# Performance work log

Hardware: AMD Instinct MI355X
Metric: run time of the kernel (lower is better)

The kernel has to match this reference:

```python
import jax, jax.numpy as jnp
import numpy as np

H = 4          # n_head
DM = 512       # d_model
DK = 512       # d_k (hardcoded in module)
NL = 32        # num_landmarks
WS = 10        # window_size
EXT = WS // 2  # ext_len = 5
T = 2 * EXT + WS  # tile width = 20


def _ln(x, g, b, eps=1e-5):
    m = jnp.mean(x, axis=-1, keepdims=True)
    v = jnp.mean((x - m) ** 2, axis=-1, keepdims=True)
    return (x - m) / jnp.sqrt(v + eps) * g + b


def setup_inputs() -> dict:
    key = jax.random.key(0)
    ks = jax.random.split(key, 8)
    b, s = 8, 2000
    inp = {
        "X": jax.random.normal(ks[0], (b, s, DM), dtype=jnp.float32),
        "event_emb": jnp.zeros((1,), jnp.float32),
        "g": jnp.zeros((1,), jnp.float32),
        "mask": jnp.ones((b, s, 1), jnp.float32),
        "Wq": 0.02 * jax.random.normal(ks[1], (DM, H * DK), jnp.float32),
        "bq": jnp.zeros((H * DK,), jnp.float32),
        "Wk": 0.02 * jax.random.normal(ks[2], (DM, H * DK), jnp.float32),
        "bk": jnp.zeros((H * DK,), jnp.float32),
        "Wv": 0.02 * jax.random.normal(ks[3], (DM, H * DK), jnp.float32),
        "bv": jnp.zeros((H * DK,), jnp.float32),
        "Wo": 0.02 * jax.random.normal(ks[4], (H * DK, DM), jnp.float32),
        "bo": jnp.zeros((DM,), jnp.float32),
        "Wd": 0.02 * jax.random.normal(ks[5], (DM, H * NL), jnp.float32),
        "bd": jnp.zeros((H * NL,), jnp.float32),
        "lnl_g": jnp.ones((H * DK,), jnp.float32),
        "lnl_b": jnp.zeros((H * DK,), jnp.float32),
        "lns_g": jnp.ones((H * DK,), jnp.float32),
        "lns_b": jnp.zeros((H * DK,), jnp.float32),
    }
    return inp


def reference(X, event_emb, g, mask, Wq, bq, Wk, bk, Wv, bv, Wo, bo, Wd, bd,
              lnl_g, lnl_b, lns_g, lns_b):
    b, s, _ = X.shape
    G = s // WS  # number of windows
    scale = 1.0 / np.sqrt(DK)

    def split(x):  # [b,s,H*DK] -> [b,H,s,DK]
        return x.reshape(b, s, H, DK).transpose(0, 2, 1, 3)

    Q = split(X @ Wq + bq) * scale
    K = split(_ln(X @ Wk + bk, lnl_g, lnl_b))
    V = split(_ln(X @ Wv + bv, lnl_g, lnl_b))

    pad_mask = mask[..., 0] == 0  # [b,s] True where padded

    # landmark (Nystrom-style) compression
    hs = X @ Wd + bd  # [b,s,H*NL]
    hs = jnp.where(pad_mask[:, :, None], -jnp.inf, hs)
    hs = jax.nn.softmax(hs.astype(jnp.float32), axis=1).astype(X.dtype)
    hs = hs.reshape(b, s, H, NL).transpose(0, 2, 3, 1)  # [b,H,NL,s]
    K_c = jnp.einsum('bhls,bhsd->bhld', hs, K)  # [b,H,NL,DK]
    V_c = jnp.einsum('bhls,bhsd->bhld', hs, V)
    # dual_ln_s over flattened heads
    K_c = _ln(K_c.transpose(0, 2, 1, 3).reshape(b, NL, H * DK), lns_g, lns_b)
    K_c = K_c.reshape(b, NL, H, DK).transpose(0, 2, 1, 3)
    V_c = _ln(V_c.transpose(0, 2, 1, 3).reshape(b, NL, H * DK), lns_g, lns_b)
    V_c = V_c.reshape(b, NL, H, DK).transpose(0, 2, 1, 3)

    attn_compress = jnp.einsum('bhsd,bhld->bhsl', Q, K_c)  # [b,H,s,NL]

    # sliding-window chunked attention (v2 tiling)
    idx = jnp.arange(G)[:, None] * WS + jnp.arange(T)[None, :]  # [G,T]
    K_pad = jnp.pad(K, ((0, 0), (0, 0), (EXT, EXT), (0, 0)))
    K_tiles = K_pad[:, :, idx, :]  # [b,H,G,T,DK]
    m_pad = jnp.pad(pad_mask, ((0, 0), (EXT, EXT)), constant_values=True)
    m_tiles = m_pad[:, idx]  # [b,G,T]
    Q_tiles = Q.reshape(b, H, G, WS, DK)
    win = jnp.einsum('bhgwd,bhgtd->bhgwt', Q_tiles, K_tiles)  # [b,H,G,WS,T]
    win = jnp.where(m_tiles[:, None, :, None, :], -jnp.inf, win)
    win = win.reshape(b, H, s, T)

    scores = jnp.concatenate([attn_compress, win], axis=-1)  # [b,H,s,NL+T]
    attn = jax.nn.softmax(scores.astype(jnp.float32), axis=-1).astype(X.dtype)
    attn = jnp.where(pad_mask[:, None, :, None], 0.0, attn)

    C = jnp.einsum('bhsl,bhld->bhsd', attn[..., :NL], V_c)
    V_pad = jnp.pad(V, ((0, 0), (0, 0), (EXT, EXT), (0, 0)))
    V_tiles = V_pad[:, :, idx, :]  # [b,H,G,T,DK]
    win_p = attn[..., NL:].reshape(b, H, G, WS, T)
    C = C + jnp.einsum('bhgwt,bhgtd->bhgwd', win_p, V_tiles).reshape(b, H, s, DK)

    out = C.transpose(0, 2, 1, 3).reshape(b, s, H * DK) @ Wo + bo
    return out
```

## Files before the change

### kernel.cpp

```cpp
#include <hip/hip_runtime.h>
#include <math.h>

#define BB 8
#define SS 2000
#define DMM 512
#define HHN 4
#define DKK 512
#define HDK 2048
#define NLL 32
#define HNL 128
#define GGN 200
#define WSZ 10
#define TTN 20
#define EXTT 5
#define MMR (BB*SS)

typedef unsigned short bf16_t;
typedef __attribute__((ext_vector_type(8))) short short8;
typedef __attribute__((ext_vector_type(4))) float floatx4;

#define GLL16(gp, lp) __builtin_amdgcn_global_load_lds( \
    (__attribute__((address_space(1))) void*)(gp), \
    (__attribute__((address_space(3))) void*)(lp), 16, 0, 0)

__device__ __forceinline__ float bf2f(bf16_t u) {
  union { unsigned u; float f; } x; x.u = ((unsigned)u) << 16; return x.f;
}
__device__ __forceinline__ bf16_t f2bf(float f) {
  union { float f; unsigned u; } x; x.f = f;
  unsigned r = x.u + 0x7FFFu + ((x.u >> 16) & 1u);
  return (bf16_t)(r >> 16);
}

__device__ __forceinline__ float block_sum256(float v, float* sh) {
  #pragma unroll
  for (int off = 32; off > 0; off >>= 1) v += __shfl_down(v, off);
  if ((threadIdx.x & 63) == 0) sh[threadIdx.x >> 6] = v;
  __syncthreads();
  float t = sh[0] + sh[1] + sh[2] + sh[3];
  __syncthreads();
  return t;
}

__global__ __launch_bounds__(256)
void x_to_bf16(const float* __restrict__ X, bf16_t* __restrict__ Xb) {
  int i = blockIdx.x * 256 + threadIdx.x;
  float4 a = *(const float4*)&X[(size_t)i * 8];
  float4 b = *(const float4*)&X[(size_t)i * 8 + 4];
  ushort4 u0, u1;
  u0.x = f2bf(a.x); u0.y = f2bf(a.y); u0.z = f2bf(a.z); u0.w = f2bf(a.w);
  u1.x = f2bf(b.x); u1.y = f2bf(b.y); u1.z = f2bf(b.z); u1.w = f2bf(b.w);
  *(ushort4*)&Xb[(size_t)i * 8] = u0;
  *(ushort4*)&Xb[(size_t)i * 8 + 4] = u1;
}

__global__ __launch_bounds__(256)
void transpose_w(const float* __restrict__ W, bf16_t* __restrict__ Wt,
                 int K, int N) {
  __shared__ float Ts[64][65];
  int n0 = blockIdx.x * 64, k0 = blockIdx.y * 64;
  int tid = threadIdx.x;
  #pragma unroll
  for (int i = 0; i < 16; ++i) {
    int e = i * 256 + tid;
    int r = e >> 6, c = e & 63;
    Ts[r][c] = W[(size_t)(k0 + r) * N + n0 + c];
  }
  __syncthreads();
  #pragma unroll
  for (int i = 0; i < 16; ++i) {
    int e = i * 256 + tid;
    int r = e >> 6, c = e & 63;
    Wt[(size_t)(n0 + r) * K + k0 + c] = f2bf(Ts[c][r]);
  }
}

template <typename TO>
__global__ __launch_bounds__(256)
void gemm_bf16(const bf16_t* __restrict__ A, const bf16_t* __restrict__ Bt,
               const float* __restrict__ bias, TO* __restrict__ Cout,
               int M, int N, int K, float alpha) {
  __shared__ bf16_t As[128 * 32];
  __shared__ bf16_t Bs[128 * 32];
  int tid = threadIdx.x;
  int wave = tid >> 6, lane = tid & 63;
  int wr = wave >> 1, wc = wave & 1;
  int quad = lane >> 4, ml = lane & 15;
  int bm = blockIdx.y * 128, bn = blockIdx.x * 128;

  floatx4 acc[4][4];
  #pragma unroll
  for (int i = 0; i < 4; ++i)
    #pragma unroll
    for (int j = 0; j < 4; ++j)
      #pragma unroll
      for (int r = 0; r < 4; ++r) acc[i][j][r] = 0.f;

  int lin0 = wave * 64 + lane;
  int lin1 = 256 + lin0;
  int row0 = lin0 >> 2, ch0 = (lin0 & 3) ^ ((row0 >> 1) & 3);
  int row1 = lin1 >> 2, ch1 = (lin1 & 3) ^ ((row1 >> 1) & 3);
  const bf16_t* gA0 = &A[(size_t)(bm + row0) * K + ch0 * 8];
  const bf16_t* gA1 = &A[(size_t)(bm + row1) * K + ch1 * 8];
  const bf16_t* gB0 = &Bt[(size_t)(bn + row0) * K + ch0 * 8];
  const bf16_t* gB1 = &Bt[(size_t)(bn + row1) * K + ch1 * 8];

  for (int k0 = 0; k0 < K; k0 += 32) {
    GLL16(gA0 + k0, &As[lin0 * 8]);
    GLL16(gA1 + k0, &As[lin1 * 8]);
    GLL16(gB0 + k0, &Bs[lin0 * 8]);
    GLL16(gB1 + k0, &Bs[lin1 * 8]);
    __syncthreads();
    short8 af[4], bfr[4];
    #pragma unroll
    for (int i = 0; i < 4; ++i) {
      int row = wr * 64 + i * 16 + ml;
      int sw = quad ^ ((row >> 1) & 3);
      af[i] = *(const short8*)&As[row * 32 + sw * 8];
    }
    #pragma unroll
    for (int j = 0; j < 4; ++j) {
      int row = wc * 64 + j * 16 + ml;
      int sw = quad ^ ((row >> 1) & 3);
      bfr[j] = *(const short8*)&Bs[row * 32 + sw * 8];
    }
    #pragma unroll
    for (int i = 0; i < 4; ++i)
      #pragma unroll
      for (int j = 0; j < 4; ++j)
        acc[i][j] = __builtin_amdgcn_mfma_f32_16x16x32_bf16(af[i], bfr[j], acc[i][j], 0, 0, 0);
    __syncthreads();
  }
  #pragma unroll
  for (int i = 0; i < 4; ++i) {
    int row0o = bm + wr * 64 + i * 16 + quad * 4;
    #pragma unroll
    for (int j = 0; j < 4; ++j) {
      int col = bn + wc * 64 + j * 16 + ml;
      float bv = bias[col];
      #pragma unroll
      for (int r = 0; r < 4; ++r) {
        float o = (acc[i][j][r] + bv) * alpha;
        if constexpr (sizeof(TO) == 2)
          Cout[(size_t)(row0o + r) * N + col] = f2bf(o);
        else
          Cout[(size_t)(row0o + r) * N + col] = o;
      }
    }
  }
}

__global__ __launch_bounds__(256)
void gemm_qkv(const bf16_t* __restrict__ A, const bf16_t* __restrict__ Bt,
              const float* __restrict__ bq, const float* __restrict__ bk,
              const float* __restrict__ bv, bf16_t* __restrict__ Qo,
              bf16_t* __restrict__ Ko, bf16_t* __restrict__ Vo, float scale) {
  const int K = 512;
  __shared__ bf16_t As[128 * 32];
  __shared__ bf16_t Bs[128 * 32];
  int tid = threadIdx.x;
  int wave = tid >> 6, lane = tid & 63;
  int wr = wave >> 1, wc = wave & 1;
  int quad = lane >> 4, ml = lane & 15;
  int bm = blockIdx.y * 128, bn = blockIdx.x * 128;
  int nb = bn >> 11;
  const float* bias = nb == 0 ? bq : (nb == 1 ? bk : bv);
  bf16_t* Cout = nb == 0 ? Qo : (nb == 1 ? Ko : Vo);
  float alpha = nb == 0 ? scale : 1.f;
  int bcol = bn & 2047;

  floatx4 acc[4][4];
  #pragma unroll
  for (int i = 0; i < 4; ++i)
    #pragma unroll
    for (int j = 0; j < 4; ++j)
      #pragma unroll
      for (int r = 0; r < 4; ++r) acc[i][j][r] = 0.f;

  int lin0 = wave * 64 + lane;
  int lin1 = 256 + lin0;
  int row0 = lin0 >> 2, ch0 = (lin0 & 3) ^ ((row0 >> 1) & 3);
  int row1 = lin1 >> 2, ch1 = (lin1 & 3) ^ ((row1 >> 1) & 3);
  const bf16_t* gA0 = &A[(size_t)(bm + row0) * K + ch0 * 8];
  const bf16_t* gA1 = &A[(size_t)(bm + row1) * K + ch1 * 8];
  const bf16_t* gB0 = &Bt[(size_t)(bn + row0) * K + ch0 * 8];
  const bf16_t* gB1 = &Bt[(size_t)(bn + row1) * K + ch1 * 8];

  for (int k0 = 0; k0 < K; k0 += 32) {
    GLL16(gA0 + k0, &As[lin0 * 8]);
    GLL16(gA1 + k0, &As[lin1 * 8]);
    GLL16(gB0 + k0, &Bs[lin0 * 8]);
    GLL16(gB1 + k0, &Bs[lin1 * 8]);
    __syncthreads();
    short8 af[4], bfr[4];
    #pragma unroll
    for (int i = 0; i < 4; ++i) {
      int row = wr * 64 + i * 16 + ml;
      int sw = quad ^ ((row >> 1) & 3);
      af[i] = *(const short8*)&As[row * 32 + sw * 8];
    }
    #pragma unroll
    for (int j = 0; j < 4; ++j) {
      int row = wc * 64 + j * 16 + ml;
      int sw = quad ^ ((row >> 1) & 3);
      bfr[j] = *(const short8*)&Bs[row * 32 + sw * 8];
    }
    #pragma unroll
    for (int i = 0; i < 4; ++i)
      #pragma unroll
      for (int j = 0; j < 4; ++j)
        acc[i][j] = __builtin_amdgcn_mfma_f32_16x16x32_bf16(af[i], bfr[j], acc[i][j], 0, 0, 0);
    __syncthreads();
  }
  #pragma unroll
  for (int i = 0; i < 4; ++i) {
    int row0o = bm + wr * 64 + i * 16 + quad * 4;
    #pragma unroll
    for (int j = 0; j < 4; ++j) {
      int col = bcol + wc * 64 + j * 16 + ml;
      float bv2 = bias[col];
      #pragma unroll
      for (int r = 0; r < 4; ++r) {
        float o = (acc[i][j][r] + bv2) * alpha;
        Cout[(size_t)(row0o + r) * HDK + col] = f2bf(o);
      }
    }
  }
}

__global__ __launch_bounds__(256)
void ln2048_bf16(bf16_t* __restrict__ Y, const float* __restrict__ gam,
                 const float* __restrict__ bet) {
  __shared__ float sh[4];
  bf16_t* y = Y + (size_t)blockIdx.x * HDK;
  int t = threadIdx.x;
  ushort4 ra = *(const ushort4*)&y[t * 8];
  ushort4 rb = *(const ushort4*)&y[t * 8 + 4];
  float v[8];
  v[0] = bf2f(ra.x); v[1] = bf2f(ra.y); v[2] = bf2f(ra.z); v[3] = bf2f(ra.w);
  v[4] = bf2f(rb.x); v[5] = bf2f(rb.y); v[6] = bf2f(rb.z); v[7] = bf2f(rb.w);
  float s = 0.f;
  #pragma unroll
  for (int j = 0; j < 8; ++j) s += v[j];
  s = block_sum256(s, sh);
  float mean = s * (1.f / 2048.f);
  float ss = 0.f;
  #pragma unroll
  for (int j = 0; j < 8; ++j) { float d = v[j] - mean; ss = fmaf(d, d, ss); }
  ss = block_sum256(ss, sh);
  float rstd = rsqrtf(ss * (1.f / 2048.f) + 1e-5f);
  float gg[8], bb[8];
  *(float4*)&gg[0] = *(const float4*)&gam[t * 8];
  *(float4*)&gg[4] = *(const float4*)&gam[t * 8 + 4];
  *(float4*)&bb[0] = *(const float4*)&bet[t * 8];
  *(float4*)&bb[4] = *(const float4*)&bet[t * 8 + 4];
  ushort4 oa, ob;
  oa.x = f2bf((v[0] - mean) * rstd * gg[0] + bb[0]);
  oa.y = f2bf((v[1] - mean) * rstd * gg[1] + bb[1]);
  oa.z = f2bf((v[2] - mean) * rstd * gg[2] + bb[2]);
  oa.w = f2bf((v[3] - mean) * rstd * gg[3] + bb[3]);
  ob.x = f2bf((v[4] - mean) * rstd * gg[4] + bb[4]);
  ob.y = f2bf((v[5] - mean) * rstd * gg[5] + bb[5]);
  ob.z = f2bf((v[6] - mean) * rstd * gg[6] + bb[6]);
  ob.w = f2bf((v[7] - mean) * rstd * gg[7] + bb[7]);
  *(ushort4*)&y[t * 8] = oa;
  *(ushort4*)&y[t * 8 + 4] = ob;
}

__global__ __launch_bounds__(256)
void hs_colsum(const float* __restrict__ hs, const float* __restrict__ mask,
               float* __restrict__ Ssum) {
  __shared__ float red[128];
  int b = blockIdx.x / 100;
  int chunk = blockIdx.x % 100;
  int tid = threadIdx.x;
  int c = tid & 127, half = tid >> 7;
  int s0 = chunk * 20;
  float sum = 0.f;
  #pragma unroll
  for (int i = 0; i < 10; ++i) {
    int s = s0 + i * 2 + half;
    float m = mask[(size_t)b * SS + s];
    float v = hs[((size_t)b * SS + s) * HNL + c];
    sum += (m != 0.f) ? __expf(v) : 0.f;
  }
  if (half == 1) red[c] = sum;
  __syncthreads();
  if (half == 0) atomicAdd(&Ssum[b * HNL + c], sum + red[c]);
}

__global__ __launch_bounds__(256)
void compress_mfma(const bf16_t* __restrict__ Kf, const bf16_t* __restrict__ Vf,
                   const float* __restrict__ hs, const float* __restrict__ mask,
                   const float* __restrict__ Ssum, float* __restrict__ Kc,
                   float* __restrict__ Vc) {
  int dch = blockIdx.x & 3;
  int sch = (blockIdx.x >> 2) & 7;
  int bh  = blockIdx.x >> 5;
  int h = bh & 3, b = bh >> 2;
  int sbase = sch * 250;
  int dbase = dch * 128;

  __shared__ __align__(16) bf16_t Ah[32 * 40];
  __shared__ __align__(16) bf16_t Kt[128 * 40];
  __shared__ __align__(16) bf16_t Vt[128 * 40];

  int tid = threadIdx.x;
  int wave = tid >> 6, lane = tid & 63;
  int tensor = wave >> 1, nh = wave & 1;
  int quad = lane >> 4, ml = lane & 15;

  float inv8[8];
  if (tid < 128) {
    int l0 = (tid & 3) * 8;
    #pragma unroll
    for (int j = 0; j < 8; ++j)
      inv8[j] = 1.f / Ssum[b * HNL + h * NLL + l0 + j];
  }

  floatx4 acc[2][4];
  #pragma unroll
  for (int i = 0; i < 2; ++i)
    #pragma unroll
    for (int j = 0; j < 4; ++j)
      #pragma unroll
      for (int r = 0; r < 4; ++r) acc[i][j][r] = 0.f;

  for (int ks = 0; ks < 8; ++ks) {
    int s0 = ks * 32;
    if (tid < 128) {
      int si = tid >> 2;
      int l0 = (tid & 3) * 8;
      int s_l = s0 + si;
      float w[8];
      #pragma unroll
      for (int j = 0; j < 8; ++j) w[j] = 0.f;
      if (s_l < 250) {
        float m = mask[(size_t)b * SS + sbase + s_l];
        if (m != 0.f) {
          const float* p = &hs[((size_t)b * SS + sbase + s_l) * HNL + h * NLL + l0];
          float4 f0 = *(const float4*)p;
          float4 f1 = *(const float4*)(p + 4);
          w[0] = __expf(f0.x) * inv8[0];
          w[1] = __expf(f0.y) * inv8[1];
          w[2] = __expf(f0.z) * inv8[2];
          w[3] = __expf(f0.w) * inv8[3];
          w[4] = __expf(f1.x) * inv8[4];
          w[5] = __expf(f1.y) * inv8[5];
          w[6] = __expf(f1.z) * inv8[6];
          w[7] = __expf(f1.w) * inv8[7];
        }
      }
      #pragma unroll
      for (int j = 0; j < 8; ++j)
        Ah[(l0 + j) * 40 + si] = f2bf(w[j]);
    }
    {
      int si = tid >> 3;
      int d0 = (tid & 7) * 16;
      int s_l = s0 + si;
      uint4 ka = {0, 0, 0, 0}, kb = {0, 0, 0, 0};
      uint4 va = {0, 0, 0, 0}, vb = {0, 0, 0, 0};
      if (s_l < 250) {
        size_t gof = ((size_t)b * SS + sbase + s_l) * HDK + h * DKK + dbase + d0;
        ka = *(const uint4*)&Kf[gof];
        kb = *(const uint4*)&Kf[gof + 8];
        va = *(const uint4*)&Vf[gof];
        vb = *(const uint4*)&Vf[gof + 8];
      }
      const ushort* kp = (const ushort*)&ka;
      const ushort* kq = (const ushort*)&kb;
      const ushort* vp = (const ushort*)&va;
      const ushort* vq = (const ushort*)&vb;
      #pragma unroll
      for (int j = 0; j < 8; ++j) {
        Kt[(d0 + j) * 40 + si]     = kp[j];
        Kt[(d0 + 8 + j) * 40 + si] = kq[j];
        Vt[(d0 + j) * 40 + si]     = vp[j];
        Vt[(d0 + 8 + j) * 40 + si] = vq[j];
      }
    }
    __syncthreads();
    const bf16_t* Bsel = tensor ? Vt : Kt;
    #pragma unroll
    for (int i = 0; i < 2; ++i) {
      short8 af = *(const short8*)&Ah[(i * 16 + ml) * 40 + quad * 8];
      #pragma unroll
      for (int j = 0; j < 4; ++j) {
        short8 bfr = *(const short8*)&Bsel[(nh * 64 + j * 16 + ml) * 40 + quad * 8];
        acc[i][j] = __builtin_amdgcn_mfma_f32_16x16x32_bf16(af, bfr, acc[i][j], 0, 0, 0);
      }
    }
    __syncthreads();
  }
  float* outp = tensor ? Vc : Kc;
  size_t obase = ((size_t)b * 4 + h) * (NLL * DKK);
  #pragma unroll
  for (int i = 0; i < 2; ++i) {
    #pragma unroll
    for (int j = 0; j < 4; ++j) {
      int d = dbase + nh * 64 + j * 16 + ml;
      #pragma unroll
      for (int r = 0; r < 4; ++r) {
        int l = i * 16 + quad * 4 + r;
        atomicAdd(&outp[obase + (size_t)l * DKK + d], acc[i][j][r]);
      }
    }
  }
}

__global__ __launch_bounds__(256)
void ln_comp_out(const float* __restrict__ Y, const float* __restrict__ gam,
                 const float* __restrict__ bet, bf16_t* __restrict__ outp,
                 int transposed) {
  __shared__ float sh[4];
  int b = blockIdx.x >> 5, l = blockIdx.x & 31;
  size_t base = (size_t)b * 65536 + (size_t)l * 512;
  float v[8]; float s = 0.f;
  #pragma unroll
  for (int j = 0; j < 8; ++j) {
    int f = threadIdx.x + 256 * j;
    int hh = f >> 9, dd = f & 511;
    v[j] = Y[base + (size_t)hh * 16384 + dd];
    s += v[j];
  }
  s = block_sum256(s, sh);
  float mean = s * (1.f / 2048.f);
  float ss = 0.f;
  #pragma unroll
  for (int j = 0; j < 8; ++j) { float d = v[j] - mean; ss = fmaf(d, d, ss); }
  ss = block_sum256(ss, sh);
  float rstd = rsqrtf(ss * (1.f / 2048.f) + 1e-5f);
  #pragma unroll
  for (int j = 0; j < 8; ++j) {
    int f = threadIdx.x + 256 * j;
    int hh = f >> 9, dd = f & 511;
    float o = (v[j] - mean) * rstd * gam[f] + bet[f];
    if (!transposed)
      outp[(((size_t)b * 4 + hh) * 32 + l) * 512 + dd] = f2bf(o);
    else
      outp[(((size_t)b * 4 + hh) * 512 + dd) * 32 + l] = f2bf(o);
  }
}

__global__ __launch_bounds__(256)
void attn_mfma3(const bf16_t* __restrict__ Qf, const bf16_t* __restrict__ Kf,
                const bf16_t* __restrict__ Vf, const bf16_t* __restrict__ KcB,
                const bf16_t* __restrict__ VcT, const float* __restrict__ mask,
                bf16_t* __restrict__ Cf) {
  int gp = blockIdx.x % 100;
  int bh = blockIdx.x / 100;
  int h = bh & 3, b = bh >> 2;
  int g0row = gp * 20;
  int wbase = g0row - EXTT;

  __shared__ bf16_t VwT[128 * 40];
  __shared__ bf16_t Vst[30 * 136];
  __shared__ float  sc[20][68];
  __shared__ bf16_t Ps[32 * 88];
  __shared__ float  cv[32];

  int tid = threadIdx.x;
  int wave = tid >> 6, lane = tid & 63;
  int quad = lane >> 4, ml = lane & 15;

  if (tid < 30) {
    int j = wbase + tid;
    cv[tid] = (j >= 0 && j < SS && mask[(size_t)b * SS + j] != 0.f) ? 1.f : 0.f;
  }
  for (int i = tid; i < 32 * 88; i += 256) Ps[i] = 0;

  int qr0 = g0row + (ml < 20 ? ml : 19);
  int r1c = 16 + ml;
  int qr1 = g0row + (r1c < 20 ? r1c : 19);
  const bf16_t* ap0 = Qf + ((size_t)b * SS + qr0) * HDK + h * DKK;
  const bf16_t* ap1 = Qf + ((size_t)b * SS + qr1) * HDK + h * DKK;
  int brow = wave * 16 + ml;
  const bf16_t* bp;
  if (brow < 32) {
    bp = KcB + ((size_t)bh * 32 + brow) * 512;
  } else {
    int j = wbase + brow - 32;
    j = j < 0 ? 0 : (j >= SS ? SS - 1 : j);
    bp = Kf + ((size_t)b * SS + j) * HDK + h * DKK;
  }
  floatx4 s0 = {0.f, 0.f, 0.f, 0.f}, s1 = {0.f, 0.f, 0.f, 0.f};
  #pragma unroll 8
  for (int ks = 0; ks < 16; ++ks) {
    short8 af0 = *(const short8*)(ap0 + ks * 32 + quad * 8);
    short8 af1 = *(const short8*)(ap1 + ks * 32 + quad * 8);
    short8 bfr = *(const short8*)(bp  + ks * 32 + quad * 8);
    s0 = __builtin_amdgcn_mfma_f32_16x16x32_bf16(af0, bfr, s0, 0, 0, 0);
    s1 = __builtin_amdgcn_mfma_f32_16x16x32_bf16(af1, bfr, s1, 0, 0, 0);
  }
  #pragma unroll
  for (int r = 0; r < 4; ++r) {
    int row0 = quad * 4 + r;
    if (row0 < 20) sc[row0][wave * 16 + ml] = s0[r];
    int row1 = 16 + quad * 4 + r;
    if (row1 < 20) sc[row1][wave * 16 + ml] = s1[r];
  }

  uint4 vr[2];
  #pragma unroll
  for (int vi = 0; vi < 2; ++vi) {
    int idx = vi * 256 + tid;
    uint4 z = {0, 0, 0, 0};
    if (idx < 480) {
      int u = idx >> 4, c8 = idx & 15;
      int j = wbase + u;
      if (j >= 0 && j < SS)
        z = *(const uint4*)&Vf[((size_t)b * SS + j) * HDK + h * DKK + c8 * 8];
    }
    vr[vi] = z;
  }
  __syncthreads();

  if (tid < 160) {
    int r = tid >> 3, part = tid & 7;
    float mx = -INFINITY;
    #pragma unroll
    for (int i = 0; i < 8; ++i) {
      int c = part + i * 8;
      if (c < 62) {
        float v = sc[r][c];
        bool valid;
        if (c < 32) valid = true;
        else {
          int u = c - 32;
          valid = (u < 30) && (cv[u] != 0.f) && (r < 10 ? (u < 20) : (u >= 10));
        }
        v = valid ? v : -INFINITY;
        sc[r][c] = v;
        mx = fmaxf(mx, v);
      }
    }
    mx = fmaxf(mx, __shfl_xor(mx, 1));
    mx = fmaxf(mx, __shfl_xor(mx, 2));
    mx = fmaxf(mx, __shfl_xor(mx, 4));
    float sum = 0.f;
    #pragma unroll
    for (int i = 0; i < 8; ++i) {
      int c = part + i * 8;
      if (c < 62) {
        float e = expf(sc[r][c] - mx);
        sc[r][c] = e;
        sum += e;
      }
    }
    sum += __shfl_xor(sum, 1);
    sum += __shfl_xor(sum, 2);
    sum += __shfl_xor(sum, 4);
    float qm = mask[(size_t)b * SS + g0row + r];
    float inv = (qm != 0.f) ? 1.f / sum : 0.f;
    #pragma unroll
    for (int i = 0; i < 8; ++i) {
      int c = part + i * 8;
      if (c < 62) {
        float p = sc[r][c] * inv;
        if (c < 32) Ps[r * 88 + c] = f2bf(p);
        else        Ps[r * 88 + 40 + (c - 32)] = f2bf(p);
      }
    }
  }
  #pragma unroll
  for (int vi = 0; vi < 2; ++vi) {
    int idx = vi * 256 + tid;
    if (idx < 480) {
      int u = idx >> 4, c8 = idx & 15;
      *(uint4*)&Vst[u * 136 + c8 * 8] = vr[vi];
    }
  }
  __syncthreads();

  short8 pac0 = *(const short8*)&Ps[ml * 88 + quad * 8];
  short8 pac1 = *(const short8*)&Ps[(16 + ml) * 88 + quad * 8];
  short8 paw0 = *(const short8*)&Ps[ml * 88 + 40 + quad * 8];
  short8 paw1 = *(const short8*)&Ps[(16 + ml) * 88 + 40 + quad * 8];
  size_t vctbase = ((size_t)bh * 512) * 32;
  size_t cbase = ((size_t)b * SS + g0row) * HDK + h * DKK;

  #pragma unroll
  for (int ch = 0; ch < 4; ++ch) {
    int dA = ch * 128 + (wave * 2 + 0) * 16 + ml;
    int dB = ch * 128 + (wave * 2 + 1) * 16 + ml;
    short8 vcfA = *(const short8*)&VcT[vctbase + (size_t)dA * 32 + quad * 8];
    short8 vcfB = *(const short8*)&VcT[vctbase + (size_t)dB * 32 + quad * 8];
    if (ch < 3) {
      #pragma unroll
      for (int vi = 0; vi < 2; ++vi) {
        int idx = vi * 256 + tid;
        uint4 z = {0, 0, 0, 0};
        if (idx < 480) {
          int u = idx >> 4, c8 = idx & 15;
          int j = wbase + u;
          if (j >= 0 && j < SS)
            z = *(const uint4*)&Vf[((size_t)b * SS + j) * HDK + h * DKK + (ch + 1) * 128 + c8 * 8];
        }
        vr[vi] = z;
      }
    }
    #pragma unroll
    for (int g = 0; g < 16; ++g) {
      int gid = g * 4 + wave;
      int d0 = (gid & 7) * 16, u0 = (gid >> 3) * 4;
      int u = u0 + quad, dl = d0 + ml;
      bf16_t v = (u < 30) ? Vst[u * 136 + dl] : (bf16_t)0;
      VwT[dl * 40 + u] = v;
    }
    __syncthreads();

    #pragma unroll
    for (int half = 0; half < 2; ++half) {
      int d = ch * 128 + (wave * 2 + half) * 16 + ml;
      int dl = d - ch * 128;
      short8 vcf = half ? vcfB : vcfA;
      short8 vwf = *(const short8*)&VwT[dl * 40 + quad * 8];
      floatx4 o0 = {0.f, 0.f, 0.f, 0.f}, o1 = {0.f, 0.f, 0.f, 0.f};
      o0 = __builtin_amdgcn_mfma_f32_16x16x32_bf16(pac0, vcf, o0, 0, 0, 0);
      o0 = __builtin_amdgcn_mfma_f32_16x16x32_bf16(paw0, vwf, o0, 0, 0, 0);
      o1 = __builtin_amdgcn_mfma_f32_16x16x32_bf16(pac1, vcf, o1, 0, 0, 0);
      o1 = __builtin_amdgcn_mfma_f32_16x16x32_bf16(paw1, vwf, o1, 0, 0, 0);
      #pragma unroll
      for (int r = 0; r < 4; ++r) {
        int row0 = quad * 4 + r;
        if (row0 < 20) Cf[cbase + (size_t)row0 * HDK + d] = f2bf(o0[r]);
        int row1 = 16 + quad * 4 + r;
        if (row1 < 20) Cf[cbase + (size_t)row1 * HDK + d] = f2bf(o1[r]);
      }
    }
    if (ch < 3) {
      #pragma unroll
      for (int vi = 0; vi < 2; ++vi) {
        int idx = vi * 256 + tid;
        if (idx < 480) {
          int u = idx >> 4, c8 = idx & 15;
          *(uint4*)&Vst[u * 136 + c8 * 8] = vr[vi];
        }
      }
    }
    __syncthreads();
  }
}

extern "C" void kernel_launch(void* const* d_in, const int* in_sizes, int n_in,
                              void* d_out, int out_size, void* d_ws, size_t ws_size,
                              hipStream_t stream) {
  const float* X     = (const float*)d_in[0];
  const float* mask  = (const float*)d_in[3];
  const float* Wq    = (const float*)d_in[4];
  const float* bq    = (const float*)d_in[5];
  const float* Wk    = (const float*)d_in[6];
  const float* bk    = (const float*)d_in[7];
  const float* Wv    = (const float*)d_in[8];
  const float* bv    = (const float*)d_in[9];
  const float* Wo    = (const float*)d_in[10];
  const float* bo    = (const float*)d_in[11];
  const float* Wd    = (const float*)d_in[12];
  const float* bd    = (const float*)d_in[13];
  const float* lnl_g = (const float*)d_in[14];
  const float* lnl_b = (const float*)d_in[15];
  const float* lns_g = (const float*)d_in[16];
  const float* lns_b = (const float*)d_in[17];
  float* out = (float*)d_out;

  char* ws = (char*)d_ws;
  bf16_t* Q   = (bf16_t*)(ws);
  bf16_t* K   = (bf16_t*)(ws + 65536000);
  bf16_t* V   = (bf16_t*)(ws + 131072000);
  float*  hs  = (float*) (ws + 196608000);
  float*  Kc  = (float*) (ws + 204800000);
  float*  Vc  = (float*) (ws + 206897152);
  bf16_t* C   = Q;
  bf16_t* Wqt = (bf16_t*)(ws + 196608000);
  bf16_t* Wkt = (bf16_t*)(ws + 196608000 + 2097152);
  bf16_t* Wvt = (bf16_t*)(ws + 196608000 + 4194304);
  bf16_t* Wdt = (bf16_t*)(ws + 204800000);
  bf16_t* Wot = (bf16_t*)(ws + 65536000);
  bf16_t* KcB = (bf16_t*)(ws + 196608000);
  bf16_t* VcT = (bf16_t*)(ws + 196608000 + 1048576);
  float*  Ssum = (float*)d_out;
  bf16_t* Xbf  = (bf16_t*)((char*)d_out + 65536);

  const float scale = 0.04419417382415922f;
  const dim3 blk(256);

  x_to_bf16<<<4000, blk, 0, stream>>>(X, Xbf);
  transpose_w<<<dim3(32, 8), blk, 0, stream>>>(Wq, Wqt, 512, 2048);
  transpose_w<<<dim3(32, 8), blk, 0, stream>>>(Wk, Wkt, 512, 2048);
  transpose_w<<<dim3(32, 8), blk, 0, stream>>>(Wv, Wvt, 512, 2048);
  transpose_w<<<dim3(2, 8),  blk, 0, stream>>>(Wd, Wdt, 512, 128);
  gemm_qkv<<<dim3(48, 125), blk, 0, stream>>>(Xbf, Wqt, bq, bk, bv, Q, K, V, scale);
  gemm_bf16<float><<<dim3(1, 125), blk, 0, stream>>>(Xbf, Wdt, bd, hs, MMR, 128, 512, 1.f);
  hipMemsetAsync(d_out, 0, BB * HNL * sizeof(float), stream);
  ln2048_bf16<<<MMR, blk, 0, stream>>>(K, lnl_g, lnl_b);
  ln2048_bf16<<<MMR, blk, 0, stream>>>(V, lnl_g, lnl_b);
  hs_colsum<<<BB * 100, blk, 0, stream>>>(hs, mask, Ssum);
  hipMemsetAsync(ws + 204800000, 0, 4194304, stream);
  compress_mfma<<<1024, blk, 0, stream>>>(K, V, hs, mask, Ssum, Kc, Vc);
  ln_comp_out<<<BB * NLL, blk, 0, stream>>>(Kc, lns_g, lns_b, KcB, 0);
  ln_comp_out<<<BB * NLL, blk, 0, stream>>>(Vc, lns_g, lns_b, VcT, 1);
  attn_mfma3<<<BB * HHN * 100, blk, 0, stream>>>(Q, K, V, KcB, VcT, mask, C);
  transpose_w<<<dim3(8, 32), blk, 0, stream>>>(Wo, Wot, 2048, 512);
  gemm_bf16<float><<<dim3(4, 125), blk, 0, stream>>>(C, Wot, bo, out, MMR, 512, 2048, 1.f);
}
```

Baseline: 530.8 us.

## Fuse QKV and landmark GEMMs, merge LN launches, drop attention V transpose

Merges the three Q/K/V weight transposes into one kernel and folds the landmark projection into the QKV GEMM as a 49th column block, writing fp32 hs. The two LayerNorm passes over K and V become one launch, as do the two compressed-output LayerNorm kernels. In the attention kernel, the LDS transpose of the V window and its barrier are replaced by an XOR-swizzled staging buffer that each lane gathers from directly. The goal is fewer launches and less LDS traffic and synchronisation, at the cost of scalar LDS gathers and weights staged in the output buffer.

```diff
diff --git a/kernel.cpp b/kernel.cpp
--- a/kernel.cpp
+++ b/kernel.cpp
@@ -75,6 +75,31 @@
   }
 }
 
+__global__ __launch_bounds__(256)
+void transpose_wqkv(const float* __restrict__ Wq, const float* __restrict__ Wk,
+                    const float* __restrict__ Wv, bf16_t* __restrict__ Wt) {
+  __shared__ float Ts[64][65];
+  int by = blockIdx.y;
+  int which = by >> 3;
+  const float* W = which == 0 ? Wq : (which == 1 ? Wk : Wv);
+  int k0 = (by & 7) * 64;
+  int n0 = blockIdx.x * 64;
+  int tid = threadIdx.x;
+  #pragma unroll
+  for (int i = 0; i < 16; ++i) {
+    int e = i * 256 + tid;
+    int r = e >> 6, c = e & 63;
+    Ts[r][c] = W[(size_t)(k0 + r) * 2048 + n0 + c];
+  }
+  __syncthreads();
+  #pragma unroll
+  for (int i = 0; i < 16; ++i) {
+    int e = i * 256 + tid;
+    int r = e >> 6, c = e & 63;
+    Wt[(size_t)(which * 2048 + n0 + r) * 512 + k0 + c] = f2bf(Ts[c][r]);
+  }
+}
+
 template <typename TO>
 __global__ __launch_bounds__(256)
 void gemm_bf16(const bf16_t* __restrict__ A, const bf16_t* __restrict__ Bt,
@@ -151,10 +176,11 @@
 }
 
 __global__ __launch_bounds__(256)
-void gemm_qkv(const bf16_t* __restrict__ A, const bf16_t* __restrict__ Bt,
-              const float* __restrict__ bq, const float* __restrict__ bk,
-              const float* __restrict__ bv, bf16_t* __restrict__ Qo,
-              bf16_t* __restrict__ Ko, bf16_t* __restrict__ Vo, float scale) {
+void gemm_qkvh(const bf16_t* __restrict__ A, const bf16_t* __restrict__ Bt,
+               const float* __restrict__ bq, const float* __restrict__ bk,
+               const float* __restrict__ bv, const float* __restrict__ bd,
+               bf16_t* __restrict__ Qo, bf16_t* __restrict__ Ko,
+               bf16_t* __restrict__ Vo, float* __restrict__ hso, float scale) {
   const int K = 512;
   __shared__ bf16_t As[128 * 32];
   __shared__ bf16_t Bs[128 * 32];
@@ -164,8 +190,8 @@
   int quad = lane >> 4, ml = lane & 15;
   int bm = blockIdx.y * 128, bn = blockIdx.x * 128;
   int nb = bn >> 11;
-  const float* bias = nb == 0 ? bq : (nb == 1 ? bk : bv);
-  bf16_t* Cout = nb == 0 ? Qo : (nb == 1 ? Ko : Vo);
+  const float* bias = nb == 0 ? bq : (nb == 1 ? bk : (nb == 2 ? bv : bd));
+  bf16_t* Cb = nb == 0 ? Qo : (nb == 1 ? Ko : Vo);
   float alpha = nb == 0 ? scale : 1.f;
   int bcol = bn & 2047;
 
@@ -222,7 +248,8 @@
       #pragma unroll
       for (int r = 0; r < 4; ++r) {
         float o = (acc[i][j][r] + bv2) * alpha;
-        Cout[(size_t)(row0o + r) * HDK + col] = f2bf(o);
+        if (nb == 3) hso[(size_t)(row0o + r) * HNL + col] = o;
+        else         Cb[(size_t)(row0o + r) * HDK + col] = f2bf(o);
       }
     }
   }
@@ -410,11 +437,15 @@
 }
 
 __global__ __launch_bounds__(256)
-void ln_comp_out(const float* __restrict__ Y, const float* __restrict__ gam,
-                 const float* __restrict__ bet, bf16_t* __restrict__ outp,
-                 int transposed) {
+void ln_comp_both(const float* __restrict__ Kc, const float* __restrict__ Vc,
+                  const float* __restrict__ gam, const float* __restrict__ bet,
+                  bf16_t* __restrict__ KcB, bf16_t* __restrict__ VcT) {
   __shared__ float sh[4];
-  int b = blockIdx.x >> 5, l = blockIdx.x & 31;
+  int which = blockIdx.x >> 8;
+  int bid = blockIdx.x & 255;
+  const float* Y = which ? Vc : Kc;
+  bf16_t* outp = which ? VcT : KcB;
+  int b = bid >> 5, l = bid & 31;
   size_t base = (size_t)b * 65536 + (size_t)l * 512;
   float v[8]; float s = 0.f;
   #pragma unroll
@@ -436,7 +467,7 @@
     int f = threadIdx.x + 256 * j;
     int hh = f >> 9, dd = f & 511;
     float o = (v[j] - mean) * rstd * gam[f] + bet[f];
-    if (!transposed)
+    if (!which)
       outp[(((size_t)b * 4 + hh) * 32 + l) * 512 + dd] = f2bf(o);
     else
       outp[(((size_t)b * 4 + hh) * 512 + dd) * 32 + l] = f2bf(o);
@@ -444,7 +475,7 @@
 }
 
 __global__ __launch_bounds__(256)
-void attn_mfma3(const bf16_t* __restrict__ Qf, const bf16_t* __restrict__ Kf,
+void attn_mfma4(const bf16_t* __restrict__ Qf, const bf16_t* __restrict__ Kf,
                 const bf16_t* __restrict__ Vf, const bf16_t* __restrict__ KcB,
                 const bf16_t* __restrict__ VcT, const float* __restrict__ mask,
                 bf16_t* __restrict__ Cf) {
@@ -454,8 +485,7 @@
   int g0row = gp * 20;
   int wbase = g0row - EXTT;
 
-  __shared__ bf16_t VwT[128 * 40];
-  __shared__ bf16_t Vst[30 * 136];
+  __shared__ bf16_t Vst[30 * 128];
   __shared__ float  sc[20][68];
   __shared__ bf16_t Ps[32 * 88];
   __shared__ float  cv[32];
@@ -568,7 +598,8 @@
     int idx = vi * 256 + tid;
     if (idx < 480) {
       int u = idx >> 4, c8 = idx & 15;
-      *(uint4*)&Vst[u * 136 + c8 * 8] = vr[vi];
+      int slot = c8 ^ ((u >> 3) & 3);
+      *(uint4*)&Vst[u * 128 + slot * 8] = vr[vi];
     }
   }
   __syncthreads();
@@ -600,22 +631,24 @@
         vr[vi] = z;
       }
     }
-    #pragma unroll
-    for (int g = 0; g < 16; ++g) {
-      int gid = g * 4 + wave;
-      int d0 = (gid & 7) * 16, u0 = (gid >> 3) * 4;
-      int u = u0 + quad, dl = d0 + ml;
-      bf16_t v = (u < 30) ? Vst[u * 136 + dl] : (bf16_t)0;
-      VwT[dl * 40 + u] = v;
-    }
-    __syncthreads();
 
     #pragma unroll
     for (int half = 0; half < 2; ++half) {
-      int d = ch * 128 + (wave * 2 + half) * 16 + ml;
-      int dl = d - ch * 128;
+      int dl = (wave * 2 + half) * 16 + ml;
+      int d = ch * 128 + dl;
+      int cd = dl >> 3, de = dl & 7;
+      short8 vwf;
+      #pragma unroll
+      for (int j = 0; j < 8; ++j) {
+        int u = quad * 8 + j;
+        bf16_t x = 0;
+        if (u < 30) {
+          int slot = cd ^ ((u >> 3) & 3);
+          x = Vst[u * 128 + slot * 8 + de];
+        }
+        vwf[j] = (short)x;
+      }
       short8 vcf = half ? vcfB : vcfA;
-      short8 vwf = *(const short8*)&VwT[dl * 40 + quad * 8];
       floatx4 o0 = {0.f, 0.f, 0.f, 0.f}, o1 = {0.f, 0.f, 0.f, 0.f};
       o0 = __builtin_amdgcn_mfma_f32_16x16x32_bf16(pac0, vcf, o0, 0, 0, 0);
       o0 = __builtin_amdgcn_mfma_f32_16x16x32_bf16(paw0, vwf, o0, 0, 0, 0);
@@ -629,17 +662,19 @@
         if (row1 < 20) Cf[cbase + (size_t)row1 * HDK + d] = f2bf(o1[r]);
       }
     }
+    __syncthreads();
     if (ch < 3) {
       #pragma unroll
       for (int vi = 0; vi < 2; ++vi) {
         int idx = vi * 256 + tid;
         if (idx < 480) {
           int u = idx >> 4, c8 = idx & 15;
-          *(uint4*)&Vst[u * 136 + c8 * 8] = vr[vi];
+          int slot = c8 ^ ((u >> 3) & 3);
+          *(uint4*)&Vst[u * 128 + slot * 8] = vr[vi];
         }
       }
-    }
-    __syncthreads();
+      __syncthreads();
+    }
   }
 }
 
@@ -672,35 +707,29 @@
   float*  Kc  = (float*) (ws + 204800000);
   float*  Vc  = (float*) (ws + 206897152);
   bf16_t* C   = Q;
-  bf16_t* Wqt = (bf16_t*)(ws + 196608000);
-  bf16_t* Wkt = (bf16_t*)(ws + 196608000 + 2097152);
-  bf16_t* Wvt = (bf16_t*)(ws + 196608000 + 4194304);
-  bf16_t* Wdt = (bf16_t*)(ws + 204800000);
   bf16_t* Wot = (bf16_t*)(ws + 65536000);
   bf16_t* KcB = (bf16_t*)(ws + 196608000);
   bf16_t* VcT = (bf16_t*)(ws + 196608000 + 1048576);
-  float*  Ssum = (float*)d_out;
-  bf16_t* Xbf  = (bf16_t*)((char*)d_out + 65536);
+  float*  Ssum  = (float*)d_out;
+  bf16_t* Xbf   = (bf16_t*)((char*)d_out + 65536);
+  bf16_t* Wqkvt = (bf16_t*)((char*)d_out + 16449536);
+  bf16_t* Wdt   = (bf16_t*)((char*)d_out + 22740992);
 
   const float scale = 0.04419417382415922f;
   const dim3 blk(256);
 
   x_to_bf16<<<4000, blk, 0, stream>>>(X, Xbf);
-  transpose_w<<<dim3(32, 8), blk, 0, stream>>>(Wq, Wqt, 512, 2048);
-  transpose_w<<<dim3(32, 8), blk, 0, stream>>>(Wk, Wkt, 512, 2048);
-  transpose_w<<<dim3(32, 8), blk, 0, stream>>>(Wv, Wvt, 512, 2048);
-  transpose_w<<<dim3(2, 8),  blk, 0, stream>>>(Wd, Wdt, 512, 128);
-  gemm_qkv<<<dim3(48, 125), blk, 0, stream>>>(Xbf, Wqt, bq, bk, bv, Q, K, V, scale);
-  gemm_bf16<float><<<dim3(1, 125), blk, 0, stream>>>(Xbf, Wdt, bd, hs, MMR, 128, 512, 1.f);
+  transpose_wqkv<<<dim3(32, 24), blk, 0, stream>>>(Wq, Wk, Wv, Wqkvt);
+  transpose_w<<<dim3(2, 8), blk, 0, stream>>>(Wd, Wdt, 512, 128);
+  gemm_qkvh<<<dim3(49, 125), blk, 0, stream>>>(Xbf, Wqkvt, bq, bk, bv, bd,
+                                               Q, K, V, hs, scale);
   hipMemsetAsync(d_out, 0, BB * HNL * sizeof(float), stream);
-  ln2048_bf16<<<MMR, blk, 0, stream>>>(K, lnl_g, lnl_b);
-  ln2048_bf16<<<MMR, blk, 0, stream>>>(V, lnl_g, lnl_b);
+  ln2048_bf16<<<2 * MMR, blk, 0, stream>>>(K, lnl_g, lnl_b);
   hs_colsum<<<BB * 100, blk, 0, stream>>>(hs, mask, Ssum);
   hipMemsetAsync(ws + 204800000, 0, 4194304, stream);
   compress_mfma<<<1024, blk, 0, stream>>>(K, V, hs, mask, Ssum, Kc, Vc);
-  ln_comp_out<<<BB * NLL, blk, 0, stream>>>(Kc, lns_g, lns_b, KcB, 0);
-  ln_comp_out<<<BB * NLL, blk, 0, stream>>>(Vc, lns_g, lns_b, VcT, 1);
-  attn_mfma3<<<BB * HHN * 100, blk, 0, stream>>>(Q, K, V, KcB, VcT, mask, C);
+  ln_comp_both<<<512, blk, 0, stream>>>(Kc, Vc, lns_g, lns_b, KcB, VcT);
+  attn_mfma4<<<BB * HHN * 100, blk, 0, stream>>>(Q, K, V, KcB, VcT, mask, C);
   transpose_w<<<dim3(8, 32), blk, 0, stream>>>(Wo, Wot, 2048, 512);
   gemm_bf16<float><<<dim3(4, 125), blk, 0, stream>>>(C, Wot, bo, out, MMR, 512, 2048, 1.f);
 }
```

After: 527.2 us. No clear change (-0.7%).
